# Kernel optimization log

Hardware: AMD Instinct MI355X
Metric: run time of the kernel (lower is better)

## Reference

```python
import jax, jax.numpy as jnp
import numpy as np

N = 262144   # number of samples
C = 16       # GMM components
D = 64       # feature dim


def setup_inputs() -> dict:
    key = jax.random.key(0)
    k1, k2, k3, k4 = jax.random.split(key, 4)
    inputs = jax.random.normal(k1, (N, D), dtype=jnp.float32)
    # SPD inverse covariances, as produced by inverting fitted GMM covariances
    R = jax.random.normal(k2, (C, D, D), dtype=jnp.float32)
    covariances_inv = jnp.einsum('cij,ckj->cik', R, R) / D + 0.1 * jnp.eye(D, dtype=jnp.float32)
    means = jax.random.normal(k3, (C, D), dtype=jnp.float32)
    w = jax.random.uniform(k4, (C,), dtype=jnp.float32, minval=0.1, maxval=1.0)
    weights = w / jnp.sum(w)  # mixture weights sum to 1
    return {"inputs": inputs, "covariances_inv": covariances_inv,
            "means": means, "weights": weights}


def reference(inputs, covariances_inv, means, weights):
    # Mahalanobis quadratic form per component: d[n,c] = (x_n - m_c)^T Sigma_c^{-1} (x_n - m_c)
    centered = inputs[:, None, :] - means[None, :, :]                # [N, C, D]
    distances_sqr = jnp.einsum('ncd,cde,nce->nc', centered, covariances_inv, centered)  # [N, C]
    # score_n = prod_c d[n,c] ** w_c
    score = jnp.prod(distances_sqr ** weights[None, :], axis=1)      # [N]
    return score
```

## Files before the change

kernel.cpp:

```cpp
#include <hip/hip_runtime.h>

typedef __attribute__((ext_vector_type(4))) float f32x4;
typedef __attribute__((ext_vector_type(8))) short bf16x8;

__device__ __forceinline__ short f2bf(float f) {
    union { float f; unsigned u; } v; v.f = f;
    unsigned u = v.u;
    u += 0x7FFFu + ((u >> 16) & 1u);
    return (short)(u >> 16);
}

__device__ __forceinline__ int pack_bf2(float a, float b) {
    union { float f; unsigned u; } ua, ub; ua.f = a; ub.f = b;
    unsigned x = ua.u + 0x8000u, y = ub.u + 0x8000u;
    return (int)__builtin_amdgcn_perm(y, x, 0x07060302u);
}

__global__ void gmm_prep(const float* __restrict__ Ainv,
                         const float* __restrict__ means,
                         short* __restrict__ AbP,
                         short* __restrict__ Bneg2,
                         float* __restrict__ kscal) {
    __shared__ float sA[64 * 68];
    __shared__ float sm[64];
    __shared__ float sb[64];
    const int c = blockIdx.x, t = threadIdx.x;
    const float* A = Ainv + c * 4096;
    #pragma unroll
    for (int i = 0; i < 4; ++i) {
        int flat = i * 1024 + t * 4;
        int r = flat >> 6, col = flat & 63;
        *(f32x4*)&sA[r * 68 + col] = *(const f32x4*)(A + flat);
    }
    if (t < 64) sm[t] = means[c * 64 + t];
    __syncthreads();
    {
        int j = t >> 2, seg = t & 3;
        float p = 0.f;
        #pragma unroll
        for (int k = 0; k < 16; ++k) p += sA[j * 68 + seg * 16 + k] * sm[seg * 16 + k];
        p += __shfl_xor(p, 1, 64); p += __shfl_xor(p, 2, 64);
        if ((t & 3) == 0) sb[j] = p;
    }
    __syncthreads();
    if (t < 64) {
        float km = sm[t] * sb[t];
        #pragma unroll
        for (int off = 32; off >= 1; off >>= 1) km += __shfl_xor(km, off, 64);
        if (t == 0) kscal[c] = km;
        Bneg2[c * 64 + t] = f2bf(-2.f * sb[t]);
    }
    {
        int p_ = t >> 2, kq = (t & 3) * 16;
        int rt = p_ >> 4, qh = (p_ >> 2) & 3, r = p_ & 3;
        int pj = (rt >> 1) * 32 + 8 * qh + 4 * (rt & 1) + r;
        bf16x8 v0, v1;
        #pragma unroll
        for (int i = 0; i < 8; ++i) {
            v0[i] = f2bf(sA[pj * 68 + kq + i]);
            v1[i] = f2bf(sA[pj * 68 + kq + 8 + i]);
        }
        *(bf16x8*)(AbP + c * 4096 + p_ * 64 + kq)     = v0;
        *(bf16x8*)(AbP + c * 4096 + p_ * 64 + kq + 8) = v1;
    }
}

__global__ __launch_bounds__(256, 2) void gmm_main(
    const float* __restrict__ X,
    const float* __restrict__ weights,
    const short* __restrict__ AbP,
    const short* __restrict__ Bneg2,
    const float* __restrict__ kscal,
    float* __restrict__ out) {

    __shared__ float sPart[8 * 4 * 16];

    const int tid = threadIdx.x;
    const int lane = tid & 63, w = tid >> 6;
    const int q = lane >> 4, ln = lane & 15;

    bf16x8 af[4][4][2];
    const short* Aw = AbP + (w * 4) * 4096 + ln * 64 + q * 8;
    #pragma unroll
    for (int c4 = 0; c4 < 4; ++c4)
        #pragma unroll
        for (int rt = 0; rt < 4; ++rt)
            #pragma unroll
            for (int kc = 0; kc < 2; ++kc)
                af[c4][rt][kc] = *(const bf16x8*)(Aw + c4 * 4096 + rt * 1024 + kc * 32);

    bf16x8 ab[2];
    {
        bf16x8 z;
        #pragma unroll
        for (int i = 0; i < 8; ++i) z[i] = 0;
        ab[0] = z; ab[1] = z;
        if (ln < 4) {
            ab[0] = *(const bf16x8*)(Bneg2 + (w * 4 + ln) * 64 + q * 8);
            ab[1] = *(const bf16x8*)(Bneg2 + (w * 4 + ln) * 64 + 32 + q * 8);
        }
    }
    float kw[4], wc[4];
    #pragma unroll
    for (int c4 = 0; c4 < 4; ++c4) { kw[c4] = kscal[w * 4 + c4]; wc[c4] = weights[w * 4 + c4]; }

    const int base = blockIdx.x * 512;
    const float* xp = X + (size_t)(base + ln) * 64 + q * 8;
    f32x4 xc[2][2];
    #pragma unroll
    for (int kc = 0; kc < 2; ++kc) {
        xc[kc][0] = *(const f32x4*)(xp + kc * 32);
        xc[kc][1] = *(const f32x4*)(xp + kc * 32 + 4);
    }

    const f32x4 zero4 = {0.f, 0.f, 0.f, 0.f};

    #pragma unroll 1
    for (int t = 0; t < 32; ++t) {
        const float* xnp = xp + 1024;
        f32x4 xn[2][2];
        if (t < 31) {
            #pragma unroll
            for (int kc = 0; kc < 2; ++kc) {
                xn[kc][0] = *(const f32x4*)(xnp + kc * 32);
                xn[kc][1] = *(const f32x4*)(xnp + kc * 32 + 4);
            }
        }

        bf16x8 bfr[2];
        #pragma unroll
        for (int kc = 0; kc < 2; ++kc) {
            union { int i[4]; bf16x8 v; } u;
            u.i[0] = pack_bf2(xc[kc][0][0], xc[kc][0][1]);
            u.i[1] = pack_bf2(xc[kc][0][2], xc[kc][0][3]);
            u.i[2] = pack_bf2(xc[kc][1][0], xc[kc][1][1]);
            u.i[3] = pack_bf2(xc[kc][1][2], xc[kc][1][3]);
            bfr[kc] = u.v;
        }

        f32x4 bacc = __builtin_amdgcn_mfma_f32_16x16x32_bf16(ab[0], bfr[0], zero4, 0, 0, 0);
        bacc = __builtin_amdgcn_mfma_f32_16x16x32_bf16(ab[1], bfr[1], bacc, 0, 0, 0);

        float slog = 0.f;
        #pragma unroll
        for (int c4 = 0; c4 < 4; ++c4) {
            float dp = 0.f;
            #pragma unroll
            for (int rt = 0; rt < 4; ++rt) {
                f32x4 acc = __builtin_amdgcn_mfma_f32_16x16x32_bf16(
                    af[c4][rt][0], bfr[0], zero4, 0, 0, 0);
                acc = __builtin_amdgcn_mfma_f32_16x16x32_bf16(
                    af[c4][rt][1], bfr[1], acc, 0, 0, 0);
                f32x4 xm = xc[rt >> 1][rt & 1];
                dp += acc[0] * xm[0] + acc[1] * xm[1]
                    + acc[2] * xm[2] + acc[3] * xm[3];
            }
            dp += __shfl_xor(dp, 16, 64);
            dp += __shfl_xor(dp, 32, 64);
            if (q == 0) {
                float d = dp + bacc[c4] + kw[c4];
                d = fmaxf(d, 1e-30f);
                slog += wc[c4] * __builtin_amdgcn_logf(d);
            }
        }
        if (q == 0) sPart[(t & 7) * 64 + w * 16 + ln] = slog;

        if ((t & 7) == 7) {
            __syncthreads();
            if (tid < 128) {
                int s = tid, o = (s >> 4) * 64 + (s & 15);
                float v = sPart[o] + sPart[o + 16] + sPart[o + 32] + sPart[o + 48];
                out[base + (t >> 3) * 128 + s] = __builtin_amdgcn_exp2f(v);
            }
            __syncthreads();
        }

        xp = xnp;
        #pragma unroll
        for (int kc = 0; kc < 2; ++kc) { xc[kc][0] = xn[kc][0]; xc[kc][1] = xn[kc][1]; }
    }
}

extern "C" void kernel_launch(void* const* d_in, const int* in_sizes, int n_in,
                              void* d_out, int out_size, void* d_ws, size_t ws_size,
                              hipStream_t stream) {
    const float* X       = (const float*)d_in[0];
    const float* Ainv    = (const float*)d_in[1];
    const float* means   = (const float*)d_in[2];
    const float* weights = (const float*)d_in[3];
    float* out = (float*)d_out;
    const int N = in_sizes[0] / 64;

    short* AbP   = (short*)d_ws;
    short* Bneg2 = (short*)((char*)d_ws + 131072);
    float* kscal = (float*)((char*)d_ws + 133120);

    gmm_prep<<<dim3(16), dim3(256), 0, stream>>>(Ainv, means, AbP, Bneg2, kscal);
    gmm_main<<<dim3(N / 512), dim3(256), 0, stream>>>(X, weights, AbP, Bneg2, kscal, out);
}
```

Before: 144.9 us.

## Restructure GMM kernel: stream component matrices through LDS, keep samples in registers

Inverts the work split. Previously each wave held four components' bf16 matrices in registers and streamed 512 samples through them. Now each wave keeps 64 samples (as bf16 fragments) in registers, and all 16 components' matrices are streamed through shared memory in four groups with register prefetch. The linear term and constant are folded into one MFMA per sample tile with kscal as the accumulator init. The cross-wave LDS reduction is replaced by in-wave shuffles, which removes the per-8-iteration block barriers. Risks are higher LDS traffic, two barriers per group, and lower reuse of each matrix per block, since blocks now cover 256 samples and occupancy targets 3 blocks.

```diff
diff --git a/kernel.cpp b/kernel.cpp
--- a/kernel.cpp
+++ b/kernel.cpp
@@ -5,21 +5,25 @@
 
 __device__ __forceinline__ short f2bf(float f) {
     union { float f; unsigned u; } v; v.f = f;
-    unsigned u = v.u;
-    u += 0x7FFFu + ((u >> 16) & 1u);
+    unsigned u = v.u + 0x7FFFu + ((v.u >> 16) & 1u);
     return (short)(u >> 16);
 }
-
 __device__ __forceinline__ int pack_bf2(float a, float b) {
     union { float f; unsigned u; } ua, ub; ua.f = a; ub.f = b;
     unsigned x = ua.u + 0x8000u, y = ub.u + 0x8000u;
     return (int)__builtin_amdgcn_perm(y, x, 0x07060302u);
 }
+__device__ __forceinline__ float bflo(int p) {
+    union { int i; float f; } v; v.i = p << 16; return v.f;
+}
+__device__ __forceinline__ float bfhi(int p) {
+    union { int i; float f; } v; v.i = p & 0xffff0000; return v.f;
+}
 
 __global__ void gmm_prep(const float* __restrict__ Ainv,
                          const float* __restrict__ means,
-                         short* __restrict__ AbP,
-                         short* __restrict__ Bneg2,
+                         short* __restrict__ AbP16,
+                         short* __restrict__ Bb16,
                          float* __restrict__ kscal) {
     __shared__ float sA[64 * 68];
     __shared__ float sm[64];
@@ -48,136 +52,130 @@
         #pragma unroll
         for (int off = 32; off >= 1; off >>= 1) km += __shfl_xor(km, off, 64);
         if (t == 0) kscal[c] = km;
-        Bneg2[c * 64 + t] = f2bf(-2.f * sb[t]);
     }
-    {
-        int p_ = t >> 2, kq = (t & 3) * 16;
-        int rt = p_ >> 4, qh = (p_ >> 2) & 3, r = p_ & 3;
-        int pj = (rt >> 1) * 32 + 8 * qh + 4 * (rt & 1) + r;
-        bf16x8 v0, v1;
+    #pragma unroll
+    for (int rep = 0; rep < 2; ++rep) {
+        int f = rep * 256 + t;
+        int rt = f >> 7, kc = (f >> 6) & 1, L = f & 63;
+        int ln = L & 15, q = L >> 4;
+        int pj = (rt >> 1) * 32 + 8 * (ln >> 2) + 4 * (rt & 1) + (ln & 3);
+        const float* src = &sA[pj * 68 + 32 * kc + 8 * q];
+        bf16x8 v;
         #pragma unroll
-        for (int i = 0; i < 8; ++i) {
-            v0[i] = f2bf(sA[pj * 68 + kq + i]);
-            v1[i] = f2bf(sA[pj * 68 + kq + 8 + i]);
-        }
-        *(bf16x8*)(AbP + c * 4096 + p_ * 64 + kq)     = v0;
-        *(bf16x8*)(AbP + c * 4096 + p_ * 64 + kq + 8) = v1;
+        for (int j = 0; j < 8; ++j) v[j] = f2bf(src[j]);
+        *(bf16x8*)(AbP16 + c * 4096 + f * 8) = v;
+    }
+    if (t < 8) {
+        int kc = t >> 2, q = t & 3, L = q * 16 + c;
+        bf16x8 v;
+        #pragma unroll
+        for (int j = 0; j < 8; ++j) v[j] = f2bf(-2.f * sb[32 * kc + 8 * q + j]);
+        *(bf16x8*)(Bb16 + kc * 512 + L * 8) = v;
     }
 }
 
-__global__ __launch_bounds__(256, 2) void gmm_main(
+__global__ __launch_bounds__(256, 3) void gmm_main(
     const float* __restrict__ X,
     const float* __restrict__ weights,
-    const short* __restrict__ AbP,
-    const short* __restrict__ Bneg2,
+    const short* __restrict__ AbP16,
+    const short* __restrict__ Bb16,
     const float* __restrict__ kscal,
     float* __restrict__ out) {
 
-    __shared__ float sPart[8 * 4 * 16];
+    __shared__ short sAb[16384];
 
     const int tid = threadIdx.x;
     const int lane = tid & 63, w = tid >> 6;
     const int q = lane >> 4, ln = lane & 15;
+    const int base = blockIdx.x * 256 + w * 64;
+    const f32x4 zero4 = {0.f, 0.f, 0.f, 0.f};
 
-    bf16x8 af[4][4][2];
-    const short* Aw = AbP + (w * 4) * 4096 + ln * 64 + q * 8;
+    union BFrag { bf16x8 v; int i[4]; };
+    BFrag xb[4][2];
     #pragma unroll
-    for (int c4 = 0; c4 < 4; ++c4)
+    for (int t = 0; t < 4; ++t) {
+        const float* xr = X + (size_t)(base + t * 16 + ln) * 64 + 8 * q;
         #pragma unroll
-        for (int rt = 0; rt < 4; ++rt)
-            #pragma unroll
-            for (int kc = 0; kc < 2; ++kc)
-                af[c4][rt][kc] = *(const bf16x8*)(Aw + c4 * 4096 + rt * 1024 + kc * 32);
-
-    bf16x8 ab[2];
-    {
-        bf16x8 z;
-        #pragma unroll
-        for (int i = 0; i < 8; ++i) z[i] = 0;
-        ab[0] = z; ab[1] = z;
-        if (ln < 4) {
-            ab[0] = *(const bf16x8*)(Bneg2 + (w * 4 + ln) * 64 + q * 8);
-            ab[1] = *(const bf16x8*)(Bneg2 + (w * 4 + ln) * 64 + 32 + q * 8);
+        for (int kc = 0; kc < 2; ++kc) {
+            f32x4 a = *(const f32x4*)(xr + 32 * kc);
+            f32x4 b = *(const f32x4*)(xr + 32 * kc + 4);
+            xb[t][kc].i[0] = pack_bf2(a[0], a[1]);
+            xb[t][kc].i[1] = pack_bf2(a[2], a[3]);
+            xb[t][kc].i[2] = pack_bf2(b[0], b[1]);
+            xb[t][kc].i[3] = pack_bf2(b[2], b[3]);
         }
     }
-    float kw[4], wc[4];
+
+    f32x4 kw = *(const f32x4*)(kscal + 4 * q);
+    f32x4 wc4 = *(const f32x4*)(weights + 4 * q);
+    bf16x8 bb0 = *(const bf16x8*)(Bb16 + lane * 8);
+    bf16x8 bb1 = *(const bf16x8*)(Bb16 + 512 + lane * 8);
+    f32x4 lin[4];
     #pragma unroll
-    for (int c4 = 0; c4 < 4; ++c4) { kw[c4] = kscal[w * 4 + c4]; wc[c4] = weights[w * 4 + c4]; }
-
-    const int base = blockIdx.x * 512;
-    const float* xp = X + (size_t)(base + ln) * 64 + q * 8;
-    f32x4 xc[2][2];
-    #pragma unroll
-    for (int kc = 0; kc < 2; ++kc) {
-        xc[kc][0] = *(const f32x4*)(xp + kc * 32);
-        xc[kc][1] = *(const f32x4*)(xp + kc * 32 + 4);
+    for (int t = 0; t < 4; ++t) {
+        lin[t] = __builtin_amdgcn_mfma_f32_16x16x32_bf16(bb0, xb[t][0].v, kw, 0, 0, 0);
+        lin[t] = __builtin_amdgcn_mfma_f32_16x16x32_bf16(bb1, xb[t][1].v, lin[t], 0, 0, 0);
     }
 
-    const f32x4 zero4 = {0.f, 0.f, 0.f, 0.f};
+    int4 pf[8];
+    #pragma unroll
+    for (int i = 0; i < 8; ++i)
+        pf[i] = ((const int4*)AbP16)[i * 256 + tid];
+
+    float slog[4] = {0.f, 0.f, 0.f, 0.f};
 
     #pragma unroll 1
-    for (int t = 0; t < 32; ++t) {
-        const float* xnp = xp + 1024;
-        f32x4 xn[2][2];
-        if (t < 31) {
+    for (int g = 0; g < 4; ++g) {
+        #pragma unroll
+        for (int i = 0; i < 8; ++i)
+            ((int4*)sAb)[i * 256 + tid] = pf[i];
+        __syncthreads();
+        if (g < 3) {
+            const int4* src = (const int4*)(AbP16 + (g + 1) * 16384);
             #pragma unroll
-            for (int kc = 0; kc < 2; ++kc) {
-                xn[kc][0] = *(const f32x4*)(xnp + kc * 32);
-                xn[kc][1] = *(const f32x4*)(xnp + kc * 32 + 4);
+            for (int i = 0; i < 8; ++i) pf[i] = src[i * 256 + tid];
+        }
+
+        #pragma unroll
+        for (int cl = 0; cl < 4; ++cl) {
+            bf16x8 af[4][2];
+            #pragma unroll
+            for (int rt = 0; rt < 4; ++rt)
+                #pragma unroll
+                for (int kc = 0; kc < 2; ++kc)
+                    af[rt][kc] = *(const bf16x8*)&sAb[((cl * 4 + rt) * 2 + kc) * 512 + lane * 8];
+
+            #pragma unroll
+            for (int t = 0; t < 4; ++t) {
+                float dp = 0.f;
+                #pragma unroll
+                for (int rt = 0; rt < 4; ++rt) {
+                    f32x4 acc = __builtin_amdgcn_mfma_f32_16x16x32_bf16(
+                        af[rt][0], xb[t][0].v, zero4, 0, 0, 0);
+                    acc = __builtin_amdgcn_mfma_f32_16x16x32_bf16(
+                        af[rt][1], xb[t][1].v, acc, 0, 0, 0);
+                    int pa = xb[t][rt >> 1].i[(rt & 1) * 2];
+                    int pb = xb[t][rt >> 1].i[(rt & 1) * 2 + 1];
+                    dp += acc[0] * bflo(pa) + acc[1] * bfhi(pa)
+                        + acc[2] * bflo(pb) + acc[3] * bfhi(pb);
+                }
+                dp += __shfl_xor(dp, 16, 64);
+                dp += __shfl_xor(dp, 32, 64);
+                if (q == g) {
+                    float d = fmaxf(dp + lin[t][cl], 1e-30f);
+                    slog[t] = fmaf(wc4[cl], __builtin_amdgcn_logf(d), slog[t]);
+                }
             }
         }
+        __syncthreads();
+    }
 
-        bf16x8 bfr[2];
-        #pragma unroll
-        for (int kc = 0; kc < 2; ++kc) {
-            union { int i[4]; bf16x8 v; } u;
-            u.i[0] = pack_bf2(xc[kc][0][0], xc[kc][0][1]);
-            u.i[1] = pack_bf2(xc[kc][0][2], xc[kc][0][3]);
-            u.i[2] = pack_bf2(xc[kc][1][0], xc[kc][1][1]);
-            u.i[3] = pack_bf2(xc[kc][1][2], xc[kc][1][3]);
-            bfr[kc] = u.v;
-        }
-
-        f32x4 bacc = __builtin_amdgcn_mfma_f32_16x16x32_bf16(ab[0], bfr[0], zero4, 0, 0, 0);
-        bacc = __builtin_amdgcn_mfma_f32_16x16x32_bf16(ab[1], bfr[1], bacc, 0, 0, 0);
-
-        float slog = 0.f;
-        #pragma unroll
-        for (int c4 = 0; c4 < 4; ++c4) {
-            float dp = 0.f;
-            #pragma unroll
-            for (int rt = 0; rt < 4; ++rt) {
-                f32x4 acc = __builtin_amdgcn_mfma_f32_16x16x32_bf16(
-                    af[c4][rt][0], bfr[0], zero4, 0, 0, 0);
-                acc = __builtin_amdgcn_mfma_f32_16x16x32_bf16(
-                    af[c4][rt][1], bfr[1], acc, 0, 0, 0);
-                f32x4 xm = xc[rt >> 1][rt & 1];
-                dp += acc[0] * xm[0] + acc[1] * xm[1]
-                    + acc[2] * xm[2] + acc[3] * xm[3];
-            }
-            dp += __shfl_xor(dp, 16, 64);
-            dp += __shfl_xor(dp, 32, 64);
-            if (q == 0) {
-                float d = dp + bacc[c4] + kw[c4];
-                d = fmaxf(d, 1e-30f);
-                slog += wc[c4] * __builtin_amdgcn_logf(d);
-            }
-        }
-        if (q == 0) sPart[(t & 7) * 64 + w * 16 + ln] = slog;
-
-        if ((t & 7) == 7) {
-            __syncthreads();
-            if (tid < 128) {
-                int s = tid, o = (s >> 4) * 64 + (s & 15);
-                float v = sPart[o] + sPart[o + 16] + sPart[o + 32] + sPart[o + 48];
-                out[base + (t >> 3) * 128 + s] = __builtin_amdgcn_exp2f(v);
-            }
-            __syncthreads();
-        }
-
-        xp = xnp;
-        #pragma unroll
-        for (int kc = 0; kc < 2; ++kc) { xc[kc][0] = xn[kc][0]; xc[kc][1] = xn[kc][1]; }
+    #pragma unroll
+    for (int t = 0; t < 4; ++t) {
+        float tot = slog[t];
+        tot += __shfl_xor(tot, 16, 64);
+        tot += __shfl_xor(tot, 32, 64);
+        if (q == 0) out[base + t * 16 + ln] = __builtin_amdgcn_exp2f(tot);
     }
 }
 
@@ -191,10 +189,10 @@
     float* out = (float*)d_out;
     const int N = in_sizes[0] / 64;
 
-    short* AbP   = (short*)d_ws;
-    short* Bneg2 = (short*)((char*)d_ws + 131072);
+    short* AbP16 = (short*)d_ws;
+    short* Bb16  = (short*)((char*)d_ws + 131072);
     float* kscal = (float*)((char*)d_ws + 133120);
 
-    gmm_prep<<<dim3(16), dim3(256), 0, stream>>>(Ainv, means, AbP, Bneg2, kscal);
-    gmm_main<<<dim3(N / 512), dim3(256), 0, stream>>>(X, weights, AbP, Bneg2, kscal, out);
+    gmm_prep<<<dim3(16), dim3(256), 0, stream>>>(Ainv, means, AbP16, Bb16, kscal);
+    gmm_main<<<dim3(N / 256), dim3(256), 0, stream>>>(X, weights, AbP16, Bb16, kscal, out);
 }
```

Result: slower. 161.1 us (+11.2%).
